# Kernel tuning notes

Hardware: AMD Instinct MI355X
Metric: run time of the kernel (lower is better)

## Reference

```python
import jax, jax.numpy as jnp
import numpy as np

B, S, N_IN = 4, 2048, 1024
H, DK = 8, 128  # n_latent = 1024 = H * DK


def setup_inputs() -> dict:
    key = jax.random.key(0)
    ks = jax.random.split(key, 7)
    scale = 1.0 / np.sqrt(N_IN)
    return {
        "x": jax.random.normal(ks[0], (B, S, N_IN), jnp.float32),
        "Wq": jax.random.normal(ks[1], (N_IN, H * DK), jnp.float32) * scale,
        "bq": jax.random.normal(ks[2], (H * DK,), jnp.float32) * 0.01,
        "Wk": jax.random.normal(ks[3], (N_IN, H * DK), jnp.float32) * scale,
        "bk": jax.random.normal(ks[4], (H * DK,), jnp.float32) * 0.01,
        "w_fc": jax.random.normal(ks[5], (H,), jnp.float32) * (1.0 / np.sqrt(H)),
        "b_fc": jax.random.normal(ks[6], (1,), jnp.float32) * 0.01,
    }


def reference(x, Wq, bq, Wk, bk, w_fc, b_fc):
    b, s, _ = x.shape
    # projections with nonlinear gates
    Q = jnp.tanh(x @ Wq + bq).reshape(b, s, H, DK).transpose(0, 2, 1, 3)      # [B,H,S,DK]
    K = jax.nn.sigmoid(x @ Wk + bk).reshape(b, s, H, DK).transpose(0, 2, 1, 3)  # [B,H,S,DK]
    scores = jnp.einsum("bhqd,bhkd->bhqk", Q, K) / jnp.sqrt(jnp.float32(DK))  # [B,H,S,S]
    attn = jax.nn.softmax(scores, axis=-1)
    # dropout is identity in eval mode
    pooled = attn.mean(axis=-2)                    # mean over query dim -> [B,H,S]
    pooled = pooled.transpose(0, 2, 1)             # [B,S,H]
    out = pooled @ w_fc[:, None] + b_fc            # [B,S,1]
    return out
```

## Files before the change

### kernel.cpp

```cpp
#include <hip/hip_runtime.h>
#include <hip/hip_bf16.h>

constexpr int Bn  = 4;
constexpr int Sn  = 2048;
constexpr int NIN = 1024;
constexpr int Hn  = 8;
constexpr int DKn = 128;
constexpr int NL  = Hn * DKn;
constexpr int Mrows = Bn * Sn;
constexpr int KTILES = NIN / 32;

typedef __bf16 bf16x8 __attribute__((ext_vector_type(8)));
typedef float  f32x4  __attribute__((ext_vector_type(4)));

__device__ __forceinline__ unsigned short f2bf(float f) {
    unsigned u = __builtin_bit_cast(unsigned, f);
    u += 0x7FFFu + ((u >> 16) & 1u);
    return (unsigned short)(u >> 16);
}
__device__ __forceinline__ unsigned pk2(float lo, float hi) {
    return (unsigned)f2bf(lo) | ((unsigned)f2bf(hi) << 16);
}

__device__ __forceinline__ void stage16(const unsigned short* g, unsigned short* l) {
    __builtin_amdgcn_global_load_lds(
        (const __attribute__((address_space(1))) unsigned int*)g,
        (__attribute__((address_space(3))) unsigned int*)l,
        16, 0, 0);
}

__global__ void convert_x(const float* __restrict__ x, unsigned short* __restrict__ Ap)
{
    const int gid = blockIdx.x * 256 + threadIdx.x;
    const int e = gid * 8;
    const int row = e >> 10, k = e & 1023;
    const int tm = row >> 7, r = row & 127;
    const int kc = k >> 5, kk = k & 31;
    const float4 v0 = *(const float4*)&x[e];
    const float4 v1 = *(const float4*)&x[e + 4];
    uint4 w;
    w.x = pk2(v0.x, v0.y); w.y = pk2(v0.z, v0.w);
    w.z = pk2(v1.x, v1.y); w.w = pk2(v1.z, v1.w);
    const size_t tile = (size_t)(tm * KTILES + kc) * 8192;
    const int byte = (r * 64 + kk * 2) ^ ((r & 7) << 4);
    *(uint4*)((char*)Ap + tile + byte) = w;
}

__global__ void convert_w(const float* __restrict__ Wq, const float* __restrict__ Wk,
                          unsigned short* __restrict__ Bp)
{
    const int tn = blockIdx.x >> 5, kc = blockIdx.x & 31;
    const int t = threadIdx.x;
    const int c = t & 127, kh = (t >> 7) * 16;
    const float* __restrict__ W = (tn < 8) ? Wq : Wk;
    const int ncol = (tn & 7) * 128 + c;
    const int k0 = kc * 32 + kh;
    float v[16];
    #pragma unroll
    for (int j = 0; j < 16; ++j)
        v[j] = W[(size_t)(k0 + j) * NL + ncol];
    uint4 w0, w1;
    w0.x = pk2(v[0], v[1]);  w0.y = pk2(v[2], v[3]);
    w0.z = pk2(v[4], v[5]);  w0.w = pk2(v[6], v[7]);
    w1.x = pk2(v[8], v[9]);  w1.y = pk2(v[10], v[11]);
    w1.z = pk2(v[12], v[13]); w1.w = pk2(v[14], v[15]);
    const size_t tbase = (size_t)blockIdx.x * 8192;
    const int b0 = (c * 64 + kh * 2) ^ ((c & 7) << 4);
    const int b1 = (c * 64 + kh * 2 + 16) ^ ((c & 7) << 4);
    *(uint4*)((char*)Bp + tbase + b0) = w0;
    *(uint4*)((char*)Bp + tbase + b1) = w1;
}

__global__ __launch_bounds__(256) void gemm_kernel(
    const unsigned short* __restrict__ Ap, const unsigned short* __restrict__ Bp,
    const float* __restrict__ bq, const float* __restrict__ bk,
    unsigned short* __restrict__ Qb, unsigned short* __restrict__ Kb)
{
    __shared__ unsigned short Asm[128 * 32];
    __shared__ unsigned short Bsm[128 * 32];

    const int tid = threadIdx.x;
    const int wave = tid >> 6, lane = tid & 63;
    const int ln = lane & 15, kg = lane >> 4;
    const int wr = wave >> 1, wc = wave & 1;

    const int bid = blockIdx.x;
    const int wg = (bid & 7) * 128 + (bid >> 3);
    const int bm = wg >> 4, bn = wg & 15;

    const unsigned short* At = Ap + (size_t)bm * (KTILES * 4096);
    const unsigned short* Bt = Bp + (size_t)bn * (KTILES * 4096);

    f32x4 acc[4][4];
    #pragma unroll
    for (int m = 0; m < 4; ++m)
        #pragma unroll
        for (int n = 0; n < 4; ++n) acc[m][n] = (f32x4){0.f, 0.f, 0.f, 0.f};

    int aoff[4], boff[4];
    #pragma unroll
    for (int m = 0; m < 4; ++m) {
        const int row = wr * 64 + m * 16 + ln;
        aoff[m] = (row * 64 + kg * 16) ^ ((ln & 7) << 4);
        const int col = wc * 64 + m * 16 + ln;
        boff[m] = (col * 64 + kg * 16) ^ ((ln & 7) << 4);
    }

    for (int kc = 0; kc < KTILES; ++kc) {
        __syncthreads();
        const unsigned short* ga = At + kc * 4096;
        const unsigned short* gb = Bt + kc * 4096;
        stage16(ga + tid * 8,        Asm + tid * 8);
        stage16(ga + 2048 + tid * 8, Asm + 2048 + tid * 8);
        stage16(gb + tid * 8,        Bsm + tid * 8);
        stage16(gb + 2048 + tid * 8, Bsm + 2048 + tid * 8);
        __syncthreads();

        bf16x8 af[4], bfv[4];
        #pragma unroll
        for (int m = 0; m < 4; ++m) af[m] = *(const bf16x8*)((const char*)Asm + aoff[m]);
        #pragma unroll
        for (int n = 0; n < 4; ++n) bfv[n] = *(const bf16x8*)((const char*)Bsm + boff[n]);
        #pragma unroll
        for (int m = 0; m < 4; ++m)
            #pragma unroll
            for (int n = 0; n < 4; ++n)
                acc[m][n] = __builtin_amdgcn_mfma_f32_16x16x32_bf16(af[m], bfv[n], acc[m][n], 0, 0, 0);
    }

    const bool isQ = (bn < 8);
    const float* __restrict__ bias = isQ ? bq : bk;
    unsigned short* __restrict__ outp = isQ ? Qb : Kb;
    const int cbase = (isQ ? bn : bn - 8) * 128 + wc * 64 + (ln & ~3);
    float4 b4[4];
    #pragma unroll
    for (int n = 0; n < 4; ++n) b4[n] = *(const float4*)&bias[cbase + n * 16];
    const int i = ln & 3;

    #pragma unroll
    for (int m = 0; m < 4; ++m) {
        const size_t grow = bm * 128 + wr * 64 + m * 16 + kg * 4 + i;
        #pragma unroll
        for (int n = 0; n < 4; ++n) {
            float a0 = acc[m][n][0], a1 = acc[m][n][1], a2 = acc[m][n][2], a3 = acc[m][n][3];
            float t;
            t = __shfl_xor((i & 1) ? a0 : a1, 1); if (i & 1) a0 = t; else a1 = t;
            t = __shfl_xor((i & 1) ? a2 : a3, 1); if (i & 1) a2 = t; else a3 = t;
            t = __shfl_xor((i & 2) ? a0 : a2, 2); if (i & 2) a0 = t; else a2 = t;
            t = __shfl_xor((i & 2) ? a1 : a3, 2); if (i & 2) a1 = t; else a3 = t;
            a0 += b4[n].x; a1 += b4[n].y; a2 += b4[n].z; a3 += b4[n].w;
            float r0, r1, r2, r3;
            if (isQ) { r0 = tanhf(a0); r1 = tanhf(a1); r2 = tanhf(a2); r3 = tanhf(a3); }
            else {
                r0 = 1.0f / (1.0f + __expf(-a0)); r1 = 1.0f / (1.0f + __expf(-a1));
                r2 = 1.0f / (1.0f + __expf(-a2)); r3 = 1.0f / (1.0f + __expf(-a3));
            }
            uint2 w; w.x = pk2(r0, r1); w.y = pk2(r2, r3);
            *(uint2*)&outp[grow * NL + cbase + n * 16] = w;
        }
    }
}

__global__ __launch_bounds__(512, 2) void attn_kernel(
    const unsigned short* __restrict__ Qb,
    const unsigned short* __restrict__ Kb, float* __restrict__ colsum)
{
    __shared__ float lsum[64];
    const int tid  = threadIdx.x;
    const int wave = tid >> 6, lane = tid & 63;
    const int ln15 = lane & 15, lg = lane >> 4;
    const int qt = blockIdx.x, h = blockIdx.y, b = blockIdx.z;
    const int q0 = qt * 64;

    if (tid < 64) lsum[tid] = 0.0f;

    bf16x8 qf[4][4];
    #pragma unroll
    for (int t = 0; t < 4; ++t) {
        const size_t ro = ((size_t)(b * Sn + q0 + t * 16 + ln15)) * NL + h * DKn + lg * 8;
        #pragma unroll
        for (int ks = 0; ks < 4; ++ks)
            qf[t][ks] = *(const bf16x8*)(Qb + ro + ks * 32);
    }
    __syncthreads();

    const unsigned short* kb0 = Kb + (size_t)b * Sn * NL + h * DKn;
    const int keyw = wave * 256;
    const float scale = 0.08838834764831845f;

    float rs[4][4];
    #pragma unroll
    for (int t = 0; t < 4; ++t)
        #pragma unroll
        for (int j = 0; j < 4; ++j) rs[t][j] = 0.0f;

    #pragma unroll 4
    for (int f = 0; f < 16; ++f) {
        const unsigned short* kr = kb0 + (size_t)(keyw + f * 16 + ln15) * NL + lg * 8;
        bf16x8 k0 = *(const bf16x8*)(kr);
        bf16x8 k1 = *(const bf16x8*)(kr + 32);
        bf16x8 k2 = *(const bf16x8*)(kr + 64);
        bf16x8 k3 = *(const bf16x8*)(kr + 96);
        #pragma unroll
        for (int t = 0; t < 4; ++t) {
            f32x4 aA = (f32x4){0.f,0.f,0.f,0.f}, aB = (f32x4){0.f,0.f,0.f,0.f};
            aA = __builtin_amdgcn_mfma_f32_16x16x32_bf16(qf[t][0], k0, aA, 0, 0, 0);
            aB = __builtin_amdgcn_mfma_f32_16x16x32_bf16(qf[t][1], k1, aB, 0, 0, 0);
            aA = __builtin_amdgcn_mfma_f32_16x16x32_bf16(qf[t][2], k2, aA, 0, 0, 0);
            aB = __builtin_amdgcn_mfma_f32_16x16x32_bf16(qf[t][3], k3, aB, 0, 0, 0);
            const f32x4 acc = aA + aB;
            rs[t][0] += __expf(acc[0] * scale);
            rs[t][1] += __expf(acc[1] * scale);
            rs[t][2] += __expf(acc[2] * scale);
            rs[t][3] += __expf(acc[3] * scale);
        }
    }

    #pragma unroll
    for (int t = 0; t < 4; ++t)
        #pragma unroll
        for (int j = 0; j < 4; ++j) {
            float v = rs[t][j];
            v += __shfl_xor(v, 1); v += __shfl_xor(v, 2);
            v += __shfl_xor(v, 4); v += __shfl_xor(v, 8);
            if (ln15 == 0) atomicAdd(&lsum[t * 16 + lg * 4 + j], v);
        }
    __syncthreads();
    if (tid < 64) lsum[tid] = 1.0f / lsum[tid];
    __syncthreads();

    float rv[4][4];
    #pragma unroll
    for (int t = 0; t < 4; ++t)
        #pragma unroll
        for (int j = 0; j < 4; ++j) rv[t][j] = lsum[t * 16 + lg * 4 + j];

    float* cs = colsum + ((size_t)(b * Hn + h)) * Sn;
    #pragma unroll 4
    for (int f = 0; f < 16; ++f) {
        const unsigned short* kr = kb0 + (size_t)(keyw + f * 16 + ln15) * NL + lg * 8;
        bf16x8 k0 = *(const bf16x8*)(kr);
        bf16x8 k1 = *(const bf16x8*)(kr + 32);
        bf16x8 k2 = *(const bf16x8*)(kr + 64);
        bf16x8 k3 = *(const bf16x8*)(kr + 96);
        float c = 0.0f;
        #pragma unroll
        for (int t = 0; t < 4; ++t) {
            f32x4 aA = (f32x4){0.f,0.f,0.f,0.f}, aB = (f32x4){0.f,0.f,0.f,0.f};
            aA = __builtin_amdgcn_mfma_f32_16x16x32_bf16(qf[t][0], k0, aA, 0, 0, 0);
            aB = __builtin_amdgcn_mfma_f32_16x16x32_bf16(qf[t][1], k1, aB, 0, 0, 0);
            aA = __builtin_amdgcn_mfma_f32_16x16x32_bf16(qf[t][2], k2, aA, 0, 0, 0);
            aB = __builtin_amdgcn_mfma_f32_16x16x32_bf16(qf[t][3], k3, aB, 0, 0, 0);
            const f32x4 acc = aA + aB;
            c = fmaf(__expf(acc[0] * scale), rv[t][0], c);
            c = fmaf(__expf(acc[1] * scale), rv[t][1], c);
            c = fmaf(__expf(acc[2] * scale), rv[t][2], c);
            c = fmaf(__expf(acc[3] * scale), rv[t][3], c);
        }
        c += __shfl_xor(c, 16); c += __shfl_xor(c, 32);
        if (lane < 16) atomicAdd(&cs[keyw + f * 16 + ln15], c);
    }
}

__global__ void final_kernel(const float* __restrict__ colsum,
                             const float* __restrict__ w_fc,
                             const float* __restrict__ b_fc,
                             float* __restrict__ out)
{
    const int idx = blockIdx.x * 256 + threadIdx.x;
    if (idx >= Bn * Sn) return;
    const int b = idx / Sn, s = idx - b * Sn;
    float accv = b_fc[0];
    #pragma unroll
    for (int h = 0; h < Hn; ++h)
        accv += colsum[((size_t)(b * Hn + h)) * Sn + s] * w_fc[h] * (1.0f / Sn);
    out[idx] = accv;
}

extern "C" void kernel_launch(void* const* d_in, const int* in_sizes, int n_in,
                              void* d_out, int out_size, void* d_ws, size_t ws_size,
                              hipStream_t stream)
{
    const float* x    = (const float*)d_in[0];
    const float* Wq   = (const float*)d_in[1];
    const float* bq   = (const float*)d_in[2];
    const float* Wk   = (const float*)d_in[3];
    const float* bk   = (const float*)d_in[4];
    const float* w_fc = (const float*)d_in[5];
    const float* b_fc = (const float*)d_in[6];
    float* out = (float*)d_out;

    const size_t NE = (size_t)Mrows * NIN;
    unsigned short* Ap = (unsigned short*)d_ws;
    unsigned short* Bp = Ap + NE;
    unsigned short* Qb = Bp + (size_t)NIN * 2048;
    unsigned short* Kb = Qb + (size_t)Mrows * NL;
    float* colsum = (float*)(Kb + (size_t)Mrows * NL);

    hipMemsetAsync(colsum, 0, (size_t)Bn * Hn * Sn * sizeof(float), stream);

    convert_x<<<Mrows * NIN / 8 / 256, 256, 0, stream>>>(x, Ap);
    convert_w<<<16 * KTILES, 256, 0, stream>>>(Wq, Wk, Bp);
    gemm_kernel<<<(Mrows / 128) * (2048 / 128), 256, 0, stream>>>(Ap, Bp, bq, bk, Qb, Kb);
    attn_kernel<<<dim3(Sn / 64, Hn, Bn), 512, 0, stream>>>(Qb, Kb, colsum);
    final_kernel<<<(Bn * Sn + 255) / 256, 256, 0, stream>>>(colsum, w_fc, b_fc, out);
}
```

Baseline: 280.9 us.

## Fold softmax scale into Q, use exp2, and prefetch K fragments

The tanh epilogue of the Q projection now multiplies by log2(e)/sqrt(DK), so the attention kernel can call exp2f directly without a per-element scale multiply. Both key passes are fully unrolled and software-pipelined: the next K fragment is loaded while the MFMAs for the current one run. The launch bounds no longer request two blocks per CU, which gives the compiler more registers for the extra in-flight loads but may reduce occupancy. Rounding Q to bf16 after scaling changes numerics slightly.

```diff
diff --git a/kernel.cpp b/kernel.cpp
--- a/kernel.cpp
+++ b/kernel.cpp
@@ -10,6 +10,8 @@
 constexpr int Mrows = Bn * Sn;
 constexpr int KTILES = NIN / 32;
 
+#define QSCL 0.1275429916f
+
 typedef __bf16 bf16x8 __attribute__((ext_vector_type(8)));
 typedef float  f32x4  __attribute__((ext_vector_type(4)));
 
@@ -22,7 +24,7 @@
     return (unsigned)f2bf(lo) | ((unsigned)f2bf(hi) << 16);
 }
 
-__device__ __forceinline__ void stage16(const unsigned short* g, unsigned short* l) {
+__device__ __forceinline__ void stage16(const void* g, void* l) {
     __builtin_amdgcn_global_load_lds(
         (const __attribute__((address_space(1))) unsigned int*)g,
         (__attribute__((address_space(3))) unsigned int*)l,
@@ -150,8 +152,10 @@
             t = __shfl_xor((i & 2) ? a1 : a3, 2); if (i & 2) a1 = t; else a3 = t;
             a0 += b4[n].x; a1 += b4[n].y; a2 += b4[n].z; a3 += b4[n].w;
             float r0, r1, r2, r3;
-            if (isQ) { r0 = tanhf(a0); r1 = tanhf(a1); r2 = tanhf(a2); r3 = tanhf(a3); }
-            else {
+            if (isQ) {
+                r0 = tanhf(a0) * QSCL; r1 = tanhf(a1) * QSCL;
+                r2 = tanhf(a2) * QSCL; r3 = tanhf(a3) * QSCL;
+            } else {
                 r0 = 1.0f / (1.0f + __expf(-a0)); r1 = 1.0f / (1.0f + __expf(-a1));
                 r2 = 1.0f / (1.0f + __expf(-a2)); r3 = 1.0f / (1.0f + __expf(-a3));
             }
@@ -161,7 +165,7 @@
     }
 }
 
-__global__ __launch_bounds__(512, 2) void attn_kernel(
+__global__ __launch_bounds__(512) void attn_kernel(
     const unsigned short* __restrict__ Qb,
     const unsigned short* __restrict__ Kb, float* __restrict__ colsum)
 {
@@ -186,7 +190,7 @@
 
     const unsigned short* kb0 = Kb + (size_t)b * Sn * NL + h * DKn;
     const int keyw = wave * 256;
-    const float scale = 0.08838834764831845f;
+    const size_t lanoff = (size_t)ln15 * NL + lg * 8;
 
     float rs[4][4];
     #pragma unroll
@@ -194,26 +198,47 @@
         #pragma unroll
         for (int j = 0; j < 4; ++j) rs[t][j] = 0.0f;
 
-    #pragma unroll 4
+    bf16x8 ka0, ka1, ka2, ka3;
+    {
+        const unsigned short* kr = kb0 + (size_t)keyw * NL + lanoff;
+        ka0 = *(const bf16x8*)(kr);
+        ka1 = *(const bf16x8*)(kr + 32);
+        ka2 = *(const bf16x8*)(kr + 64);
+        ka3 = *(const bf16x8*)(kr + 96);
+    }
+
+    #pragma unroll
     for (int f = 0; f < 16; ++f) {
-        const unsigned short* kr = kb0 + (size_t)(keyw + f * 16 + ln15) * NL + lg * 8;
-        bf16x8 k0 = *(const bf16x8*)(kr);
-        bf16x8 k1 = *(const bf16x8*)(kr + 32);
-        bf16x8 k2 = *(const bf16x8*)(kr + 64);
-        bf16x8 k3 = *(const bf16x8*)(kr + 96);
+        bf16x8 nx0, nx1, nx2, nx3;
+        {
+            const unsigned short* kr = kb0 + (size_t)(keyw + (((f + 1) & 15) << 4)) * NL + lanoff;
+            nx0 = *(const bf16x8*)(kr);
+            nx1 = *(const bf16x8*)(kr + 32);
+            nx2 = *(const bf16x8*)(kr + 64);
+            nx3 = *(const bf16x8*)(kr + 96);
+        }
         #pragma unroll
         for (int t = 0; t < 4; ++t) {
             f32x4 aA = (f32x4){0.f,0.f,0.f,0.f}, aB = (f32x4){0.f,0.f,0.f,0.f};
-            aA = __builtin_amdgcn_mfma_f32_16x16x32_bf16(qf[t][0], k0, aA, 0, 0, 0);
-            aB = __builtin_amdgcn_mfma_f32_16x16x32_bf16(qf[t][1], k1, aB, 0, 0, 0);
-            aA = __builtin_amdgcn_mfma_f32_16x16x32_bf16(qf[t][2], k2, aA, 0, 0, 0);
-            aB = __builtin_amdgcn_mfma_f32_16x16x32_bf16(qf[t][3], k3, aB, 0, 0, 0);
+            aA = __builtin_amdgcn_mfma_f32_16x16x32_bf16(qf[t][0], ka0, aA, 0, 0, 0);
+            aB = __builtin_amdgcn_mfma_f32_16x16x32_bf16(qf[t][1], ka1, aB, 0, 0, 0);
+            aA = __builtin_amdgcn_mfma_f32_16x16x32_bf16(qf[t][2], ka2, aA, 0, 0, 0);
+            aB = __builtin_amdgcn_mfma_f32_16x16x32_bf16(qf[t][3], ka3, aB, 0, 0, 0);
             const f32x4 acc = aA + aB;
-            rs[t][0] += __expf(acc[0] * scale);
-            rs[t][1] += __expf(acc[1] * scale);
-            rs[t][2] += __expf(acc[2] * scale);
-            rs[t][3] += __expf(acc[3] * scale);
-        }
+            rs[t][0] += exp2f(acc[0]);
+            rs[t][1] += exp2f(acc[1]);
+            rs[t][2] += exp2f(acc[2]);
+            rs[t][3] += exp2f(acc[3]);
+        }
+        ka0 = nx0; ka1 = nx1; ka2 = nx2; ka3 = nx3;
+    }
+
+    {
+        const unsigned short* kr = kb0 + (size_t)keyw * NL + lanoff;
+        ka0 = *(const bf16x8*)(kr);
+        ka1 = *(const bf16x8*)(kr + 32);
+        ka2 = *(const bf16x8*)(kr + 64);
+        ka3 = *(const bf16x8*)(kr + 96);
     }
 
     #pragma unroll
@@ -236,29 +261,33 @@
         for (int j = 0; j < 4; ++j) rv[t][j] = lsum[t * 16 + lg * 4 + j];
 
     float* cs = colsum + ((size_t)(b * Hn + h)) * Sn;
-    #pragma unroll 4
+    #pragma unroll
     for (int f = 0; f < 16; ++f) {
-        const unsigned short* kr = kb0 + (size_t)(keyw + f * 16 + ln15) * NL + lg * 8;
-        bf16x8 k0 = *(const bf16x8*)(kr);
-        bf16x8 k1 = *(const bf16x8*)(kr + 32);
-        bf16x8 k2 = *(const bf16x8*)(kr + 64);
-        bf16x8 k3 = *(const bf16x8*)(kr + 96);
+        bf16x8 nx0, nx1, nx2, nx3;
+        {
+            const unsigned short* kr = kb0 + (size_t)(keyw + (((f + 1) & 15) << 4)) * NL + lanoff;
+            nx0 = *(const bf16x8*)(kr);
+            nx1 = *(const bf16x8*)(kr + 32);
+            nx2 = *(const bf16x8*)(kr + 64);
+            nx3 = *(const bf16x8*)(kr + 96);
+        }
         float c = 0.0f;
         #pragma unroll
         for (int t = 0; t < 4; ++t) {
             f32x4 aA = (f32x4){0.f,0.f,0.f,0.f}, aB = (f32x4){0.f,0.f,0.f,0.f};
-            aA = __builtin_amdgcn_mfma_f32_16x16x32_bf16(qf[t][0], k0, aA, 0, 0, 0);
-            aB = __builtin_amdgcn_mfma_f32_16x16x32_bf16(qf[t][1], k1, aB, 0, 0, 0);
-            aA = __builtin_amdgcn_mfma_f32_16x16x32_bf16(qf[t][2], k2, aA, 0, 0, 0);
-            aB = __builtin_amdgcn_mfma_f32_16x16x32_bf16(qf[t][3], k3, aB, 0, 0, 0);
+            aA = __builtin_amdgcn_mfma_f32_16x16x32_bf16(qf[t][0], ka0, aA, 0, 0, 0);
+            aB = __builtin_amdgcn_mfma_f32_16x16x32_bf16(qf[t][1], ka1, aB, 0, 0, 0);
+            aA = __builtin_amdgcn_mfma_f32_16x16x32_bf16(qf[t][2], ka2, aA, 0, 0, 0);
+            aB = __builtin_amdgcn_mfma_f32_16x16x32_bf16(qf[t][3], ka3, aB, 0, 0, 0);
             const f32x4 acc = aA + aB;
-            c = fmaf(__expf(acc[0] * scale), rv[t][0], c);
-            c = fmaf(__expf(acc[1] * scale), rv[t][1], c);
-            c = fmaf(__expf(acc[2] * scale), rv[t][2], c);
-            c = fmaf(__expf(acc[3] * scale), rv[t][3], c);
+            c = fmaf(exp2f(acc[0]), rv[t][0], c);
+            c = fmaf(exp2f(acc[1]), rv[t][1], c);
+            c = fmaf(exp2f(acc[2]), rv[t][2], c);
+            c = fmaf(exp2f(acc[3]), rv[t][3], c);
         }
         c += __shfl_xor(c, 16); c += __shfl_xor(c, 32);
         if (lane < 16) atomicAdd(&cs[keyw + f * 16 + ln15], c);
+        ka0 = nx0; ka1 = nx1; ka2 = nx2; ka3 = nx3;
     }
 }
 
```

After: 452.5 us. 1.61x slower.
